# Performance work log

Hardware: AMD Instinct MI355X
Metric: run time of the kernel (lower is better)

Reference implementation:

```python
import jax, jax.numpy as jnp
import numpy as np

T, NE, NA, OBS, D, CH, VH, ITERS = 128, 64, 8, 64, 128, 128, 256, 2
B = NE * NA  # num_actors


def setup_inputs() -> dict:
    key = jax.random.key(0)
    ks = jax.random.split(key, 16)
    rn = lambda k, shape, s=0.05: jax.random.normal(k, shape, jnp.float32) * s
    z = lambda *shape: jnp.zeros(shape, jnp.float32)
    return dict(
        hidden=z(B, D),
        obs=rn(ks[0], (T, B, OBS), 1.0),
        dones=jax.random.bernoulli(ks[1], 0.05, (T, B)),
        embed1_w=rn(ks[2], (OBS, D)), embed1_b=z(D),
        embed2_w=rn(ks[3], (D, D)), embed2_b=z(D),
        gru_Wi=rn(ks[4], (D, 3 * D)), gru_bi=z(3 * D),
        gru_Wh=rn(ks[5], (D, 3 * D)), gru_bhn=z(D),
        couple_h_w=rn(ks[6], (2 * D, CH)), couple_h_b=z(CH),
        couple_out_w=rn(ks[7], (CH, 1)), couple_out_b=z(1),
        update_h_w=rn(ks[8], (2 * D, D)), update_h_b=z(D),
        update_out_w=rn(ks[9], (D, D)), update_out_b=z(D),
        value_h1_w=rn(ks[10], (D, VH)), value_h1_b=z(VH),
        value_h2_w=rn(ks[11], (VH, VH)), value_h2_b=z(VH),
        value_out_w=rn(ks[12], (VH, 1)), value_out_b=z(1),
    )


def _gru_scan(hidden, x, dones, Wi, bi, Wh, bhn):
    # flax GRUCell math: r,z gates (no hidden bias), n gate with hidden bias.
    def step(h, xd):
        xt, dt = xd
        h = jnp.where(dt[:, None], 0.0, h)  # reset carry on done
        gi = xt @ Wi + bi                   # [B, 3D]
        gh = h @ Wh                         # [B, 3D]
        i_r, i_z, i_n = jnp.split(gi, 3, axis=-1)
        h_r, h_z, h_n = jnp.split(gh, 3, axis=-1)
        r = jax.nn.sigmoid(i_r + h_r)
        zg = jax.nn.sigmoid(i_z + h_z)
        n = jnp.tanh(i_n + r * (h_n + bhn))
        new_h = (1.0 - zg) * n + zg * h
        return new_h, new_h
    return jax.lax.scan(step, hidden, (x, dones))


def reference(hidden, obs, dones,
              embed1_w, embed1_b, embed2_w, embed2_b,
              gru_Wi, gru_bi, gru_Wh, gru_bhn,
              couple_h_w, couple_h_b, couple_out_w, couple_out_b,
              update_h_w, update_h_b, update_out_w, update_out_b,
              value_h1_w, value_h1_b, value_h2_w, value_h2_b,
              value_out_w, value_out_b):
    # observation embedding MLP
    emb = jax.nn.relu(obs @ embed1_w + embed1_b)
    emb = jax.nn.relu(emb @ embed2_w + embed2_b)
    hidden, rnn_out = _gru_scan(hidden, emb, dones, gru_Wi, gru_bi, gru_Wh, gru_bhn)

    e = rnn_out.reshape(T, NE, NA, D)
    alive = (1.0 - dones.astype(jnp.float32)).reshape(T, NE, NA)
    e = e * alive[..., None]
    identity_mask = 1.0 - jnp.eye(NA, dtype=jnp.float32)

    # split-linear trick: couple_h(concat[h_i, h_j]) == h_i @ W1 + h_j @ W2 + b
    W1, W2 = couple_h_w[:D], couple_h_w[D:]
    U1, U2 = update_h_w[:D], update_h_w[D:]

    for _ in range(ITERS):
        a_i = jnp.einsum('teid,dh->teih', e, W1)  # [T,E,A,CH]
        a_j = jnp.einsum('tejd,dh->tejh', e, W2)
        Ch = jax.nn.relu(a_i[:, :, :, None, :] + a_j[:, :, None, :, :] + couple_h_b)  # [T,E,A,A,CH]
        C = jax.nn.sigmoid(jnp.einsum('teijh,h->teij', Ch, couple_out_w[:, 0]) + couple_out_b[0])
        C = C * alive[:, :, None, :] * identity_mask[None, None, :, :]
        context = jnp.einsum('teij,tejd->teid', C, e)
        delta = jax.nn.relu(e @ U1 + context @ U2 + update_h_b)
        delta = jax.nn.relu(delta @ update_out_w + update_out_b)
        e = (e + delta) * alive[..., None]

    v = jax.nn.relu(e @ value_h1_w + value_h1_b)
    v = jax.nn.relu(v @ value_h2_w + value_h2_b)
    v = (v @ value_out_w + value_out_b)[..., 0]  # [T,E,A]
    values = v.reshape(T, B)
    return hidden, values
```

## Files before the change

kernel.cpp:

```cpp
#include <hip/hip_runtime.h>
#include <hip/hip_bf16.h>
#include <math.h>

#define T_ 128
#define NE_ 64
#define NA_ 8
#define B_ 512
#define OBS_ 64
#define D_ 128
#define CH_ 128
#define VH_ 256
#define M_ (T_*B_)

typedef __attribute__((ext_vector_type(8))) short bf16x8;
typedef __attribute__((ext_vector_type(8))) _Float16 f16x8;
typedef __attribute__((ext_vector_type(4))) float f32x4;

__device__ __forceinline__ float sigmoidf_(float x){ return 1.f/(1.f+__expf(-x)); }
__device__ __forceinline__ unsigned short f2bu(float v){
  __hip_bfloat16 b = __float2bfloat16(v);
  return __builtin_bit_cast(unsigned short, b);
}
__device__ __forceinline__ float bu2f(unsigned short u){
  return __builtin_bit_cast(float, (unsigned int)u << 16);
}
__device__ __forceinline__ unsigned short f2hu(float v){
  _Float16 h = (_Float16)v;
  return __builtin_bit_cast(unsigned short, h);
}
__device__ __forceinline__ float hu2f(unsigned short u){
  return (float)__builtin_bit_cast(_Float16, u);
}

__global__ __launch_bounds__(256)
void embgi_k(const float* __restrict__ obs,
             const ushort* __restrict__ e1wT, const float* __restrict__ e1b,
             const ushort* __restrict__ e2wT, const float* __restrict__ e2b,
             const ushort* __restrict__ gWiT, const float* __restrict__ gbi,
             ushort* __restrict__ giH)
{
  __shared__ ushort S1[128*136];
  __shared__ ushort S2[128*136];
  const int tid  = threadIdx.x;
  const int lane = tid & 63, wave = tid >> 6;
  const int wm = wave >> 1, wn = wave & 1;
  const int quad = lane >> 4, ln = lane & 15;
  const int m0 = blockIdx.x * 128;

  f32x4 acc[4][4];

  #pragma unroll
  for (int i=0;i<8;i++){
    int c4 = tid + i*256;
    int m = c4 >> 4, kf = (c4 & 15) * 4;
    float4 v = *(const float4*)&obs[(size_t)(m0+m)*OBS_ + kf];
    ushort4 h; h.x=f2hu(v.x); h.y=f2hu(v.y); h.z=f2hu(v.z); h.w=f2hu(v.w);
    *(ushort4*)&S1[m*136 + kf] = h;
  }
  #pragma unroll
  for (int i=0;i<4;i++){
    int c8 = tid + i*256;
    int n = c8 >> 3, kq = (c8 & 7)*8;
    *(uint4*)&S2[n*136 + kq] = *(const uint4*)&e1wT[(size_t)n*64 + kq];
  }
  __syncthreads();

  #pragma unroll
  for (int i=0;i<4;i++)
    #pragma unroll
    for (int j=0;j<4;j++)
      #pragma unroll
      for (int r=0;r<4;r++) acc[i][j][r] = 0.f;
  #pragma unroll
  for (int ks=0; ks<2; ks++){
    const int kq = ks*32 + quad*8;
    f16x8 af[4], bfv[4];
    #pragma unroll
    for (int mt=0;mt<4;mt++)
      af[mt] = *(const f16x8*)&S1[(wm*64 + mt*16 + ln)*136 + kq];
    #pragma unroll
    for (int nt=0;nt<4;nt++)
      bfv[nt] = *(const f16x8*)&S2[(wn*64 + nt*16 + ln)*136 + kq];
    #pragma unroll
    for (int mt=0;mt<4;mt++)
      #pragma unroll
      for (int nt=0;nt<4;nt++)
        acc[mt][nt] = __builtin_amdgcn_mfma_f32_16x16x32_f16(af[mt], bfv[nt], acc[mt][nt], 0,0,0);
  }
  __syncthreads();

  #pragma unroll
  for (int mt=0;mt<4;mt++)
    #pragma unroll
    for (int r=0;r<4;r++){
      int rl = wm*64 + mt*16 + quad*4 + r;
      #pragma unroll
      for (int nt=0;nt<4;nt++){
        int cl = wn*64 + nt*16 + ln;
        S1[rl*136 + cl] = f2hu(fmaxf(acc[mt][nt][r] + e1b[cl], 0.f));
      }
    }
  #pragma unroll
  for (int i=0;i<8;i++){
    int c8 = tid + i*256;
    int n = c8 >> 4, kq = (c8 & 15)*8;
    *(uint4*)&S2[n*136 + kq] = *(const uint4*)&e2wT[(size_t)n*128 + kq];
  }
  __syncthreads();

  #pragma unroll
  for (int i=0;i<4;i++)
    #pragma unroll
    for (int j=0;j<4;j++)
      #pragma unroll
      for (int r=0;r<4;r++) acc[i][j][r] = 0.f;
  #pragma unroll
  for (int ks=0; ks<4; ks++){
    const int kq = ks*32 + quad*8;
    f16x8 af[4], bfv[4];
    #pragma unroll
    for (int mt=0;mt<4;mt++)
      af[mt] = *(const f16x8*)&S1[(wm*64 + mt*16 + ln)*136 + kq];
    #pragma unroll
    for (int nt=0;nt<4;nt++)
      bfv[nt] = *(const f16x8*)&S2[(wn*64 + nt*16 + ln)*136 + kq];
    #pragma unroll
    for (int mt=0;mt<4;mt++)
      #pragma unroll
      for (int nt=0;nt<4;nt++)
        acc[mt][nt] = __builtin_amdgcn_mfma_f32_16x16x32_f16(af[mt], bfv[nt], acc[mt][nt], 0,0,0);
  }
  __syncthreads();

  #pragma unroll
  for (int mt=0;mt<4;mt++)
    #pragma unroll
    for (int r=0;r<4;r++){
      int rl = wm*64 + mt*16 + quad*4 + r;
      #pragma unroll
      for (int nt=0;nt<4;nt++){
        int cl = wn*64 + nt*16 + ln;
        S1[rl*136 + cl] = f2hu(fmaxf(acc[mt][nt][r] + e2b[cl], 0.f));
      }
    }

  for (int c=0; c<3; c++){
    #pragma unroll
    for (int i=0;i<8;i++){
      int c8 = tid + i*256;
      int n = c8 >> 4, kq = (c8 & 15)*8;
      *(uint4*)&S2[n*136 + kq] = *(const uint4*)&gWiT[(size_t)(c*128+n)*128 + kq];
    }
    __syncthreads();
    #pragma unroll
    for (int i=0;i<4;i++)
      #pragma unroll
      for (int j=0;j<4;j++)
        #pragma unroll
        for (int r=0;r<4;r++) acc[i][j][r] = 0.f;
    #pragma unroll
    for (int ks=0; ks<4; ks++){
      const int kq = ks*32 + quad*8;
      f16x8 af[4], bfv[4];
      #pragma unroll
      for (int mt=0;mt<4;mt++)
        af[mt] = *(const f16x8*)&S1[(wm*64 + mt*16 + ln)*136 + kq];
      #pragma unroll
      for (int nt=0;nt<4;nt++)
        bfv[nt] = *(const f16x8*)&S2[(wn*64 + nt*16 + ln)*136 + kq];
      #pragma unroll
      for (int mt=0;mt<4;mt++)
        #pragma unroll
        for (int nt=0;nt<4;nt++)
          acc[mt][nt] = __builtin_amdgcn_mfma_f32_16x16x32_f16(af[mt], bfv[nt], acc[mt][nt], 0,0,0);
    }
    __syncthreads();
    #pragma unroll
    for (int mt=0;mt<4;mt++)
      #pragma unroll
      for (int r=0;r<4;r++){
        int row = m0 + wm*64 + mt*16 + quad*4 + r;
        #pragma unroll
        for (int nt=0;nt<4;nt++){
          int cl = wn*64 + nt*16 + ln;
          giH[(size_t)row*384 + c*128 + cl] = f2hu(acc[mt][nt][r] + gbi[c*128 + cl]);
        }
      }
  }
}

__global__ __launch_bounds__(256, 1)
void upd3_k(const __hip_bfloat16* __restrict__ Xe, const __hip_bfloat16* __restrict__ bcatT,
            const float* __restrict__ chb, const float* __restrict__ cow,
            const float* __restrict__ cob,
            const __hip_bfloat16* __restrict__ uhwT, const float* __restrict__ uhb,
            const __hip_bfloat16* __restrict__ uowT, const float* __restrict__ uob,
            const int* __restrict__ dones, __hip_bfloat16* __restrict__ XeOut)
{
  __shared__ ushort S1[128*136];
  __shared__ ushort Bs[128*136];
  __shared__ ushort XcS[128*136];
  __shared__ alignas(16) float AI[32][132];
  __shared__ alignas(16) float AJ[32][132];
  __shared__ alignas(16) float cbw[CH_], cww[CH_];
  __shared__ float Cs[4][NA_][NA_];
  const int tid  = threadIdx.x;
  const int lane = tid & 63, wave = tid >> 6;
  const int wm = wave >> 1, wn = wave & 1;
  const int quad = lane >> 4, ln = lane & 15;
  const int m0 = blockIdx.x * 128;

  #pragma unroll
  for (int i=0;i<8;i++){
    int c8 = tid + i*256;
    int m = c8 >> 4, kq = (c8 & 15)*8;
    *(uint4*)&S1[m*136 + kq] = *(const uint4*)((const ushort*)Xe + (size_t)(m0+m)*128 + kq);
  }
  if (tid < 128){ cbw[tid] = chb[tid]; cww[tid] = cow[tid]; }
  const float cob0 = cob[0];
  __syncthreads();

  for (int g=0; g<4; g++){
    const int r0 = g*32;
    #pragma unroll
    for (int i=0;i<8;i++){
      int c8 = tid + i*256;
      int n = c8 >> 4, kq = (c8 & 15)*8;
      *(uint4*)&Bs[n*136 + kq] = *(const uint4*)((const ushort*)bcatT + (size_t)n*128 + kq);
    }
    __syncthreads();
    {
      f32x4 acc[2][2];
      #pragma unroll
      for (int mt=0;mt<2;mt++)
        #pragma unroll
        for (int nt=0;nt<2;nt++)
          #pragma unroll
          for (int r=0;r<4;r++) acc[mt][nt][r] = 0.f;
      #pragma unroll
      for (int ks=0; ks<4; ks++){
        const int kq = ks*32 + quad*8;
        bf16x8 af[2], bfv[2];
        #pragma unroll
        for (int mt=0;mt<2;mt++)
          af[mt] = *(const bf16x8*)&S1[(r0 + mt*16 + ln)*136 + kq];
        #pragma unroll
        for (int nt=0;nt<2;nt++)
          bfv[nt] = *(const bf16x8*)&Bs[(wave*32 + nt*16 + ln)*136 + kq];
        #pragma unroll
        for (int mt=0;mt<2;mt++)
          #pragma unroll
          for (int nt=0;nt<2;nt++)
            acc[mt][nt] = __builtin_amdgcn_mfma_f32_16x16x32_bf16(af[mt], bfv[nt], acc[mt][nt], 0,0,0);
      }
      __syncthreads();
      #pragma unroll
      for (int mt=0;mt<2;mt++)
        #pragma unroll
        for (int r=0;r<4;r++)
          #pragma unroll
          for (int nt=0;nt<2;nt++)
            AI[mt*16 + quad*4 + r][wave*32 + nt*16 + ln] = acc[mt][nt][r];
    }
    #pragma unroll
    for (int i=0;i<8;i++){
      int c8 = tid + i*256;
      int n = c8 >> 4, kq = (c8 & 15)*8;
      *(uint4*)&Bs[n*136 + kq] = *(const uint4*)((const ushort*)bcatT + (size_t)(128+n)*128 + kq);
    }
    __syncthreads();
    {
      f32x4 acc[2][2];
      #pragma unroll
      for (int mt=0;mt<2;mt++)
        #pragma unroll
        for (int nt=0;nt<2;nt++)
          #pragma unroll
          for (int r=0;r<4;r++) acc[mt][nt][r] = 0.f;
      #pragma unroll
      for (int ks=0; ks<4; ks++){
        const int kq = ks*32 + quad*8;
        bf16x8 af[2], bfv[2];
        #pragma unroll
        for (int mt=0;mt<2;mt++)
          af[mt] = *(const bf16x8*)&S1[(r0 + mt*16 + ln)*136 + kq];
        #pragma unroll
        for (int nt=0;nt<2;nt++)
          bfv[nt] = *(const bf16x8*)&Bs[(wave*32 + nt*16 + ln)*136 + kq];
        #pragma unroll
        for (int mt=0;mt<2;mt++)
          #pragma unroll
          for (int nt=0;nt<2;nt++)
            acc[mt][nt] = __builtin_amdgcn_mfma_f32_16x16x32_bf16(af[mt], bfv[nt], acc[mt][nt], 0,0,0);
      }
      #pragma unroll
      for (int mt=0;mt<2;mt++)
        #pragma unroll
        for (int r=0;r<4;r++)
          #pragma unroll
          for (int nt=0;nt<2;nt++)
            AJ[mt*16 + quad*4 + r][wave*32 + nt*16 + ln] = acc[mt][nt][r];
    }
    __syncthreads();

    {
      const int env = tid >> 6;
      const int p = tid & 63, i = p >> 3, j = p & 7;
      const float* aiR = &AI[env*8 + i][0];
      const float* ajR = &AJ[env*8 + j][0];
      float s = 0.f;
      #pragma unroll
      for (int h4=0; h4<32; h4++){
        float4 a4 = *(const float4*)&aiR[h4*4];
        float4 b4 = *(const float4*)&ajR[h4*4];
        float4 c4 = *(const float4*)&cbw[h4*4];
        float4 w4 = *(const float4*)&cww[h4*4];
        s += fmaxf(a4.x + b4.x + c4.x, 0.f) * w4.x;
        s += fmaxf(a4.y + b4.y + c4.y, 0.f) * w4.y;
        s += fmaxf(a4.z + b4.z + c4.z, 0.f) * w4.z;
        s += fmaxf(a4.w + b4.w + c4.w, 0.f) * w4.w;
      }
      float Cv = sigmoidf_(s + cob0);
      Cs[env][i][j] = (i==j) ? 0.f : Cv;
    }
    __syncthreads();

    {
      const int lr = tid >> 3;
      const int env = lr >> 3, i = lr & 7;
      const int c0 = (tid & 7) * 16;
      #pragma unroll
      for (int cc=0; cc<4; cc++){
        int d = c0 + cc*4;
        float a0=0.f, a1=0.f, a2=0.f, a3=0.f;
        #pragma unroll
        for (int j=0;j<NA_;j++){
          float c = Cs[env][i][j];
          ushort4 e4 = *(const ushort4*)&S1[(r0 + env*8 + j)*136 + d];
          a0 = fmaf(c, bu2f(e4.x), a0);
          a1 = fmaf(c, bu2f(e4.y), a1);
          a2 = fmaf(c, bu2f(e4.z), a2);
          a3 = fmaf(c, bu2f(e4.w), a3);
        }
        ushort4 o; o.x=f2bu(a0); o.y=f2bu(a1); o.z=f2bu(a2); o.w=f2bu(a3);
        *(ushort4*)&XcS[(r0 + lr)*136 + d] = o;
      }
    }
    __syncthreads();
  }

  f32x4 acc[4][4];
  #pragma unroll
  for (int i=0;i<4;i++)
    #pragma unroll
    for (int j=0;j<4;j++)
      #pragma unroll
      for (int r=0;r<4;r++) acc[i][j][r] = 0.f;

  #pragma unroll
  for (int kc=0; kc<2; kc++){
    #pragma unroll
    for (int i=0;i<8;i++){
      int c8 = tid + i*256;
      int n = c8 >> 4, kq = (c8 & 15)*8;
      *(uint4*)&Bs[n*136 + kq] = *(const uint4*)((const ushort*)uhwT + (size_t)n*256 + kc*128 + kq);
    }
    __syncthreads();
    const ushort* Ab = kc ? XcS : S1;
    #pragma unroll
    for (int ks=0; ks<4; ks++){
      const int kq = ks*32 + quad*8;
      bf16x8 af[4], bfv[4];
      #pragma unroll
      for (int mt=0;mt<4;mt++)
        af[mt] = *(const bf16x8*)&Ab[(wm*64 + mt*16 + ln)*136 + kq];
      #pragma unroll
      for (int nt=0;nt<4;nt++)
        bfv[nt] = *(const bf16x8*)&Bs[(wn*64 + nt*16 + ln)*136 + kq];
      #pragma unroll
      for (int mt=0;mt<4;mt++)
        #pragma unroll
        for (int nt=0;nt<4;nt++)
          acc[mt][nt] = __builtin_amdgcn_mfma_f32_16x16x32_bf16(af[mt], bfv[nt], acc[mt][nt], 0,0,0);
    }
    __syncthreads();
  }

  #pragma unroll
  for (int i=0;i<8;i++){
    int c8 = tid + i*256;
    int n = c8 >> 4, kq = (c8 & 15)*8;
    *(uint4*)&Bs[n*136 + kq] = *(const uint4*)((const ushort*)uowT + (size_t)n*128 + kq);
  }
  #pragma unroll
  for (int mt=0;mt<4;mt++)
    #pragma unroll
    for (int r=0;r<4;r++){
      int rl = wm*64 + mt*16 + quad*4 + r;
      #pragma unroll
      for (int nt=0;nt<4;nt++){
        int cl = wn*64 + nt*16 + ln;
        XcS[rl*136 + cl] = f2bu(fmaxf(acc[mt][nt][r] + uhb[cl], 0.f));
      }
    }
  __syncthreads();

  f32x4 acc2[4][4];
  #pragma unroll
  for (int i=0;i<4;i++)
    #pragma unroll
    for (int j=0;j<4;j++)
      #pragma unroll
      for (int r=0;r<4;r++) acc2[i][j][r] = 0.f;
  #pragma unroll
  for (int ks=0; ks<4; ks++){
    const int kq = ks*32 + quad*8;
    bf16x8 af[4], bfv[4];
    #pragma unroll
    for (int mt=0;mt<4;mt++)
      af[mt] = *(const bf16x8*)&XcS[(wm*64 + mt*16 + ln)*136 + kq];
    #pragma unroll
    for (int nt=0;nt<4;nt++)
      bfv[nt] = *(const bf16x8*)&Bs[(wn*64 + nt*16 + ln)*136 + kq];
    #pragma unroll
    for (int mt=0;mt<4;mt++)
      #pragma unroll
      for (int nt=0;nt<4;nt++)
        acc2[mt][nt] = __builtin_amdgcn_mfma_f32_16x16x32_bf16(af[mt], bfv[nt], acc2[mt][nt], 0,0,0);
  }
  #pragma unroll
  for (int mt=0;mt<4;mt++){
    #pragma unroll
    for (int r=0;r<4;r++){
      int rl = wm*64 + mt*16 + quad*4 + r;
      int row = m0 + rl;
      float al = (dones[row]!=0) ? 0.f : 1.f;
      #pragma unroll
      for (int nt=0;nt<4;nt++){
        int cl = wn*64 + nt*16 + ln;
        float v = fmaxf(acc2[mt][nt][r] + uob[cl], 0.f);
        v += bu2f(S1[rl*136 + cl]);
        v *= al;
        XeOut[(size_t)row*128 + cl] = __float2bfloat16(v);
      }
    }
  }
}

__global__ __launch_bounds__(256)
void vheadf_k(const __hip_bfloat16* __restrict__ Xe, const __hip_bfloat16* __restrict__ v1wT,
              const float* __restrict__ v1b, const __hip_bfloat16* __restrict__ v2wT,
              const float* __restrict__ v2b, const float* __restrict__ vow,
              const float* __restrict__ vob, float* __restrict__ values)
{
  __shared__ ushort S1[128*136];
  __shared__ ushort S2[128*136];
  __shared__ ushort V1[2][128*136];
  const int tid  = threadIdx.x;
  const int lane = tid & 63, wave = tid >> 6;
  const int wm = wave >> 1, wn = wave & 1;
  const int quad = lane >> 4, ln = lane & 15;
  const int m0 = blockIdx.x * 128;

  #pragma unroll
  for (int i=0;i<8;i++){
    int c8 = tid + i*256;
    int m = c8 >> 4, kq = (c8 & 15)*8;
    *(uint4*)&S1[m*136 + kq] = *(const uint4*)((const ushort*)Xe + (size_t)(m0+m)*128 + kq);
  }

  for (int h=0; h<2; h++){
    #pragma unroll
    for (int i=0;i<8;i++){
      int c8 = tid + i*256;
      int n = c8 >> 4, kq = (c8 & 15)*8;
      *(uint4*)&S2[n*136 + kq] = *(const uint4*)((const ushort*)v1wT + (size_t)(h*128+n)*128 + kq);
    }
    __syncthreads();
    f32x4 acc[4][4];
    #pragma unroll
    for (int i=0;i<4;i++)
      #pragma unroll
      for (int j=0;j<4;j++)
        #pragma unroll
        for (int r=0;r<4;r++) acc[i][j][r] = 0.f;
    #pragma unroll
    for (int ks=0; ks<4; ks++){
      const int kq = ks*32 + quad*8;
      bf16x8 af[4], bfv[4];
      #pragma unroll
      for (int mt=0;mt<4;mt++)
        af[mt] = *(const bf16x8*)&S1[(wm*64 + mt*16 + ln)*136 + kq];
      #pragma unroll
      for (int nt=0;nt<4;nt++)
        bfv[nt] = *(const bf16x8*)&S2[(wn*64 + nt*16 + ln)*136 + kq];
      #pragma unroll
      for (int mt=0;mt<4;mt++)
        #pragma unroll
        for (int nt=0;nt<4;nt++)
          acc[mt][nt] = __builtin_amdgcn_mfma_f32_16x16x32_bf16(af[mt], bfv[nt], acc[mt][nt], 0,0,0);
    }
    __syncthreads();
    #pragma unroll
    for (int mt=0;mt<4;mt++)
      #pragma unroll
      for (int r=0;r<4;r++){
        int rl = wm*64 + mt*16 + quad*4 + r;
        #pragma unroll
        for (int nt=0;nt<4;nt++){
          int cl = wn*64 + nt*16 + ln;
          V1[h][rl*136 + cl] = f2bu(fmaxf(acc[mt][nt][r] + v1b[h*128 + cl], 0.f));
        }
      }
  }

  float s[4][4];
  #pragma unroll
  for (int mt=0;mt<4;mt++)
    #pragma unroll
    for (int r=0;r<4;r++) s[mt][r] = 0.f;

  for (int oc=0; oc<2; oc++){
    f32x4 acc[4][4];
    #pragma unroll
    for (int i=0;i<4;i++)
      #pragma unroll
      for (int j=0;j<4;j++)
        #pragma unroll
        for (int r=0;r<4;r++) acc[i][j][r] = 0.f;
    for (int kh=0; kh<2; kh++){
      #pragma unroll
      for (int i=0;i<8;i++){
        int c8 = tid + i*256;
        int n = c8 >> 4, kq = (c8 & 15)*8;
        *(uint4*)&S2[n*136 + kq] = *(const uint4*)((const ushort*)v2wT + (size_t)(oc*128+n)*256 + kh*128 + kq);
      }
      __syncthreads();
      #pragma unroll
      for (int ks=0; ks<4; ks++){
        const int kq = ks*32 + quad*8;
        bf16x8 af[4], bfv[4];
        #pragma unroll
        for (int mt=0;mt<4;mt++)
          af[mt] = *(const bf16x8*)&V1[kh][(wm*64 + mt*16 + ln)*136 + kq];
        #pragma unroll
        for (int nt=0;nt<4;nt++)
          bfv[nt] = *(const bf16x8*)&S2[(wn*64 + nt*16 + ln)*136 + kq];
        #pragma unroll
        for (int mt=0;mt<4;mt++)
          #pragma unroll
          for (int nt=0;nt<4;nt++)
            acc[mt][nt] = __builtin_amdgcn_mfma_f32_16x16x32_bf16(af[mt], bfv[nt], acc[mt][nt], 0,0,0);
      }
      __syncthreads();
    }
    float v2bv[4], voww[4];
    #pragma unroll
    for (int nt=0;nt<4;nt++){
      int col = oc*128 + wn*64 + nt*16 + ln;
      v2bv[nt] = v2b[col];
      voww[nt] = vow[col];
    }
    #pragma unroll
    for (int mt=0;mt<4;mt++)
      #pragma unroll
      for (int r=0;r<4;r++){
        float p = 0.f;
        #pragma unroll
        for (int nt=0;nt<4;nt++)
          p += fmaxf(acc[mt][nt][r] + v2bv[nt], 0.f) * voww[nt];
        s[mt][r] += p;
      }
  }

  #pragma unroll
  for (int off=1; off<16; off<<=1)
    #pragma unroll
    for (int mt=0;mt<4;mt++)
      #pragma unroll
      for (int r=0;r<4;r++)
        s[mt][r] += __shfl_xor(s[mt][r], off);
  if (ln == 0){
    float add = (wn == 0) ? vob[0] : 0.f;
    #pragma unroll
    for (int mt=0;mt<4;mt++)
      #pragma unroll
      for (int r=0;r<4;r++)
        atomicAdd(&values[m0 + wm*64 + mt*16 + quad*4 + r], s[mt][r] + add);
  }
}

__global__ __launch_bounds__(512, 1)
void grum8_k(const ushort* __restrict__ gih, const float* __restrict__ hidden0,
             const int* __restrict__ dones, const float* __restrict__ gWh,
             const float* __restrict__ bhn, __hip_bfloat16* __restrict__ eb_out,
             float* __restrict__ hout)
{
  __shared__ ushort wstg[32*392];
  __shared__ ushort hb[2][16*136];
  __shared__ float  dnS[T_*4];
  const int tid  = threadIdx.x;
  const int lane = tid & 63, wave = tid >> 6;
  const int quad = lane >> 4, ln = lane & 15;
  const int r0   = blockIdx.x * 4;
  const int col  = wave*16 + ln;
  const int lnb  = ln & 12;

  dnS[tid] = (dones[(size_t)(tid>>2)*B_ + r0 + (tid&3)] != 0) ? 1.f : 0.f;
  const float bhnr = bhn[col];

  for (int i=tid; i<16*136; i+=512){ hb[0][i]=0; hb[1][i]=0; }

  f16x8 bf[3][4];
  #pragma unroll
  for (int kc=0; kc<4; kc++){
    for (int i=tid; i<32*384; i+=512){
      int kk = i/384, c = i - kk*384;
      wstg[kk*392 + c] = f2hu(gWh[(size_t)(kc*32+kk)*384 + c]);
    }
    __syncthreads();
    #pragma unroll
    for (int g=0; g<3; g++){
      int c = g*128 + col;
      ushort tmp[8];
      #pragma unroll
      for (int j=0;j<8;j++) tmp[j] = wstg[(quad*8+j)*392 + c];
      bf[g][kc] = *(const f16x8*)tmp;
    }
    __syncthreads();
  }

  float hc = hidden0[(size_t)(r0+quad)*D_ + col];
  if (dnS[quad] > 0.5f) hc = 0.f;
  hb[0][(quad*4)*136 + col] = f2hu(hc);
  __syncthreads();

  const ushort* gbase = gih + ((size_t)(r0+quad))*384;
  const size_t  gstep = (size_t)B_*384;

  float c_r, c_z, c_n;
  c_r = hu2f(gbase[col]); c_z = hu2f(gbase[col+128]); c_n = hu2f(gbase[col+256]);
  ushort aR,aZ,aN, bR,bZ,bN, cR,cZ,cN, dR,dZ,dN;
  { const ushort* gp = gbase + 1*gstep; aR = gp[col]; aZ = gp[col+128]; aN = gp[col+256]; }
  { const ushort* gp = gbase + 2*gstep; bR = gp[col]; bZ = gp[col+128]; bN = gp[col+256]; }
  { const ushort* gp = gbase + 3*gstep; cR = gp[col]; cZ = gp[col+128]; cN = gp[col+256]; }
  dR=0; dZ=0; dN=0;

  ushort pend_eu = 0;

#define GSTEP(t, IR,IZ,IN, OR,OZ,ON)                                          \
  {                                                                           \
    if ((t) > 0)                                                              \
      ((ushort*)eb_out)[((size_t)((t)-1)*B_ + r0+quad)*D_ + col] = pend_eu;   \
    { int tl = (t)+4; if (tl > T_-1) tl = T_-1;                               \
      const ushort* gp = gbase + (size_t)tl*gstep;                            \
      OR = gp[col]; OZ = gp[col+128]; ON = gp[col+256]; }                     \
    const ushort* hbuf = hb[(t)&1];                                           \
    f32x4 accA[3], accB[3];                                                   \
    _Pragma("unroll")                                                         \
    for (int g=0;g<3;g++){                                                    \
      _Pragma("unroll")                                                       \
      for (int r=0;r<4;r++){ accA[g][r]=0.f; accB[g][r]=0.f; }                \
    }                                                                         \
    _Pragma("unroll")                                                         \
    for (int ks=0; ks<2; ks++){                                               \
      f16x8 ahA = *(const f16x8*)&hbuf[lnb*136 + (2*ks  )*32 + quad*8];       \
      f16x8 ahB = *(const f16x8*)&hbuf[lnb*136 + (2*ks+1)*32 + quad*8];       \
      _Pragma("unroll")                                                       \
      for (int g=0;g<3;g++){                                                  \
        accA[g] = __builtin_amdgcn_mfma_f32_16x16x32_f16(ahA, bf[g][2*ks  ], accA[g], 0,0,0); \
        accB[g] = __builtin_amdgcn_mfma_f32_16x16x32_f16(ahB, bf[g][2*ks+1], accB[g], 0,0,0); \
      }                                                                       \
    }                                                                         \
    const float dnow  = dnS[(t)*4 + quad];                                    \
    const float dnext = ((t)+1 < T_) ? dnS[((t)+1)*4 + quad] : 0.f;           \
    float rg = sigmoidf_(c_r + accA[0][0] + accB[0][0]);                      \
    float zg = sigmoidf_(c_z + accA[1][0] + accB[1][0]);                      \
    float x  = c_n + rg*(accA[2][0] + accB[2][0] + bhnr);                     \
    float ng = 2.f/(1.f+__expf(-2.f*x)) - 1.f;                                \
    float hnew = (1.f - zg)*ng + zg*hc;                                       \
    pend_eu = f2bu(hnew*(1.f-dnow));                                          \
    float hv = (dnext > 0.5f) ? 0.f : hnew;                                   \
    hc = hv;                                                                  \
    hb[((t)+1)&1][(quad*4)*136 + col] = f2hu(hv);                             \
    asm volatile("s_waitcnt lgkmcnt(0)\n\ts_barrier" ::: "memory");           \
    c_r = hu2f(IR); c_z = hu2f(IZ); c_n = hu2f(IN);                           \
  }

  for (int t=0; t<T_; t+=4){
    GSTEP(t+0, aR,aZ,aN, dR,dZ,dN);
    GSTEP(t+1, bR,bZ,bN, aR,aZ,aN);
    GSTEP(t+2, cR,cZ,cN, bR,bZ,bN);
    GSTEP(t+3, dR,dZ,dN, cR,cZ,cN);
  }
#undef GSTEP

  ((ushort*)eb_out)[((size_t)(T_-1)*B_ + r0+quad)*D_ + col] = pend_eu;
  hout[(size_t)(r0+quad)*D_ + col] = hc;
}

__global__ __launch_bounds__(256)
void packall_k(const float* __restrict__ e1w, ushort* __restrict__ e1T,
               const float* __restrict__ e2w, ushort* __restrict__ e2T,
               const float* __restrict__ gWi, ushort* __restrict__ giT,
               const float* __restrict__ chw, __hip_bfloat16* __restrict__ bcatT,
               const float* __restrict__ uhw, __hip_bfloat16* __restrict__ uhwT,
               const float* __restrict__ uow, __hip_bfloat16* __restrict__ uowT,
               const float* __restrict__ v1w, __hip_bfloat16* __restrict__ v1wT,
               const float* __restrict__ v2w, __hip_bfloat16* __restrict__ v2wT)
{
  const int b = blockIdx.x, tid = threadIdx.x;
  if (b < 32){
    int idx = b*256 + tid;
    int n = idx >> 6, k = idx & 63;
    e1T[idx] = f2hu(e1w[k*128 + n]);
  } else if (b < 96){
    int idx = (b-32)*256 + tid;
    int n = idx >> 7, k = idx & 127;
    e2T[idx] = f2hu(e2w[k*128 + n]);
  } else if (b < 288){
    int idx = (b-96)*256 + tid;
    int n = idx >> 7, k = idx & 127;
    giT[idx] = f2hu(gWi[k*384 + n]);
  } else if (b < 416){
    int idx = (b-288)*256 + tid;
    int n = idx >> 7, k = idx & 127;
    float v = (n < 128) ? chw[k*128 + n] : chw[(128+k)*128 + (n-128)];
    bcatT[idx] = __float2bfloat16(v);
  } else if (b < 544){
    int idx = (b-416)*256 + tid;
    int r = idx >> 7, c = idx & 127;
    uhwT[c*256 + r] = __float2bfloat16(uhw[idx]);
  } else if (b < 608){
    int idx = (b-544)*256 + tid;
    int r = idx >> 7, c = idx & 127;
    uowT[c*128 + r] = __float2bfloat16(uow[idx]);
  } else if (b < 736){
    int idx = (b-608)*256 + tid;
    int r = idx >> 8, c = idx & 255;
    v1wT[c*128 + r] = __float2bfloat16(v1w[idx]);
  } else {
    int idx = (b-736)*256 + tid;
    int r = idx >> 8, c = idx & 255;
    v2wT[c*256 + r] = __float2bfloat16(v2w[idx]);
  }
}

extern "C" void kernel_launch(void* const* d_in, const int* in_sizes, int n_in,
                              void* d_out, int out_size, void* d_ws, size_t ws_size,
                              hipStream_t stream) {
  const float* hidden = (const float*)d_in[0];
  const float* obs    = (const float*)d_in[1];
  const int*   dones  = (const int*)  d_in[2];
  const float* e1w = (const float*)d_in[3];
  const float* e1b = (const float*)d_in[4];
  const float* e2w = (const float*)d_in[5];
  const float* e2b = (const float*)d_in[6];
  const float* gWi = (const float*)d_in[7];
  const float* gbi = (const float*)d_in[8];
  const float* gWh = (const float*)d_in[9];
  const float* gbhn= (const float*)d_in[10];
  const float* chw = (const float*)d_in[11];
  const float* chb = (const float*)d_in[12];
  const float* cow = (const float*)d_in[13];
  const float* cob = (const float*)d_in[14];
  const float* uhw = (const float*)d_in[15];
  const float* uhb = (const float*)d_in[16];
  const float* uow = (const float*)d_in[17];
  const float* uob = (const float*)d_in[18];
  const float* v1w = (const float*)d_in[19];
  const float* v1b = (const float*)d_in[20];
  const float* v2w = (const float*)d_in[21];
  const float* v2b = (const float*)d_in[22];
  const float* vow = (const float*)d_in[23];
  const float* vob = (const float*)d_in[24];
  (void)in_sizes; (void)n_in; (void)out_size;

  float* out_hidden = (float*)d_out;
  float* out_values = (float*)d_out + (size_t)B_*D_;

  float* ws = (float*)d_ws;
  ushort* giH   = (ushort*)(ws + 10485760);
  __hip_bfloat16* Xe = (__hip_bfloat16*)(ws + 23068672);
  ushort* wb    = (ushort*)(ws + 27262976);
  if (ws_size < (size_t)27500000 * sizeof(float)) return;

  __hip_bfloat16* bcatT = (__hip_bfloat16*)wb;
  __hip_bfloat16* uhwT  = (__hip_bfloat16*)wb + 32768;
  __hip_bfloat16* uowT  = (__hip_bfloat16*)wb + 65536;
  __hip_bfloat16* v1wT  = (__hip_bfloat16*)wb + 81920;
  __hip_bfloat16* v2wT  = (__hip_bfloat16*)wb + 114688;
  ushort* e1wT = wb + 180224;
  ushort* e2wT = wb + 188416;
  ushort* gWiT = wb + 204800;

  dim3 blk(256);
  hipMemsetAsync(out_values, 0, (size_t)M_*sizeof(float), stream);
  packall_k<<<dim3(992), blk, 0, stream>>>(
    e1w, e1wT, e2w, e2wT, gWi, gWiT,
    chw, bcatT, uhw, uhwT, uow, uowT, v1w, v1wT, v2w, v2wT);

  embgi_k<<<dim3(512), blk, 0, stream>>>(obs, e1wT, e1b, e2wT, e2b, gWiT, gbi, giH);

  grum8_k<<<dim3(128), dim3(512), 0, stream>>>(giH, hidden, dones, gWh, gbhn, Xe, out_hidden);

  for (int it=0; it<2; it++){
    upd3_k<<<dim3(512), blk, 0, stream>>>(Xe, bcatT, chb, cow, cob,
                                          uhwT, uhb, uowT, uob, dones, Xe);
  }
  vheadf_k<<<dim3(512), blk, 0, stream>>>(Xe, v1wT, v1b, v2wT, v2b, vow, vob, out_values);
}
```

Baseline: 359.9 us.

## Fuse both message-passing iterations and value head into one kernel

Merges the two upd3_k launches and the vheadf_k launch into a single postgru_k kernel. Each block keeps its 128-row entity tile resident in LDS across both iterations and the value head, so the intermediate Xe tensor no longer round-trips through global memory. Shared memory is reorganized into a pooled buffer aliased between XcS/AI/AJ and V1 to fit. The risk is higher LDS footprint and register pressure, and the kernel still pays for two launches' worth of work in a single launch of 512 blocks.

```diff
diff --git a/kernel.cpp b/kernel.cpp
--- a/kernel.cpp
+++ b/kernel.cpp
@@ -190,18 +190,20 @@
 }
 
 __global__ __launch_bounds__(256, 1)
-void upd3_k(const __hip_bfloat16* __restrict__ Xe, const __hip_bfloat16* __restrict__ bcatT,
-            const float* __restrict__ chb, const float* __restrict__ cow,
-            const float* __restrict__ cob,
-            const __hip_bfloat16* __restrict__ uhwT, const float* __restrict__ uhb,
-            const __hip_bfloat16* __restrict__ uowT, const float* __restrict__ uob,
-            const int* __restrict__ dones, __hip_bfloat16* __restrict__ XeOut)
+void postgru_k(const __hip_bfloat16* __restrict__ Xe, const __hip_bfloat16* __restrict__ bcatT,
+               const float* __restrict__ chb, const float* __restrict__ cow,
+               const float* __restrict__ cob,
+               const __hip_bfloat16* __restrict__ uhwT, const float* __restrict__ uhb,
+               const __hip_bfloat16* __restrict__ uowT, const float* __restrict__ uob,
+               const int* __restrict__ dones,
+               const __hip_bfloat16* __restrict__ v1wT, const float* __restrict__ v1b,
+               const __hip_bfloat16* __restrict__ v2wT, const float* __restrict__ v2b,
+               const float* __restrict__ vow, const float* __restrict__ vob,
+               float* __restrict__ values)
 {
   __shared__ ushort S1[128*136];
   __shared__ ushort Bs[128*136];
-  __shared__ ushort XcS[128*136];
-  __shared__ alignas(16) float AI[32][132];
-  __shared__ alignas(16) float AJ[32][132];
+  __shared__ alignas(16) ushort Pool[2*128*136];
   __shared__ alignas(16) float cbw[CH_], cww[CH_];
   __shared__ float Cs[4][NA_][NA_];
   const int tid  = threadIdx.x;
@@ -210,6 +212,10 @@
   const int quad = lane >> 4, ln = lane & 15;
   const int m0 = blockIdx.x * 128;
 
+  ushort* XcS = Pool;
+  float (*AI)[132] = (float(*)[132])(Pool + 128*136);
+  float (*AJ)[132] = (float(*)[132])((char*)(Pool + 128*136) + 16896);
+
   #pragma unroll
   for (int i=0;i<8;i++){
     int c8 = tid + i*256;
@@ -220,160 +226,259 @@
   const float cob0 = cob[0];
   __syncthreads();
 
-  for (int g=0; g<4; g++){
-    const int r0 = g*32;
+  for (int it=0; it<2; it++){
+    for (int g=0; g<4; g++){
+      const int r0 = g*32;
+      #pragma unroll
+      for (int i=0;i<8;i++){
+        int c8 = tid + i*256;
+        int n = c8 >> 4, kq = (c8 & 15)*8;
+        *(uint4*)&Bs[n*136 + kq] = *(const uint4*)((const ushort*)bcatT + (size_t)n*128 + kq);
+      }
+      __syncthreads();
+      {
+        f32x4 acc[2][2];
+        #pragma unroll
+        for (int mt=0;mt<2;mt++)
+          #pragma unroll
+          for (int nt=0;nt<2;nt++)
+            #pragma unroll
+            for (int r=0;r<4;r++) acc[mt][nt][r] = 0.f;
+        #pragma unroll
+        for (int ks=0; ks<4; ks++){
+          const int kq = ks*32 + quad*8;
+          bf16x8 af[2], bfv[2];
+          #pragma unroll
+          for (int mt=0;mt<2;mt++)
+            af[mt] = *(const bf16x8*)&S1[(r0 + mt*16 + ln)*136 + kq];
+          #pragma unroll
+          for (int nt=0;nt<2;nt++)
+            bfv[nt] = *(const bf16x8*)&Bs[(wave*32 + nt*16 + ln)*136 + kq];
+          #pragma unroll
+          for (int mt=0;mt<2;mt++)
+            #pragma unroll
+            for (int nt=0;nt<2;nt++)
+              acc[mt][nt] = __builtin_amdgcn_mfma_f32_16x16x32_bf16(af[mt], bfv[nt], acc[mt][nt], 0,0,0);
+        }
+        __syncthreads();
+        #pragma unroll
+        for (int mt=0;mt<2;mt++)
+          #pragma unroll
+          for (int r=0;r<4;r++)
+            #pragma unroll
+            for (int nt=0;nt<2;nt++)
+              AI[mt*16 + quad*4 + r][wave*32 + nt*16 + ln] = acc[mt][nt][r];
+      }
+      #pragma unroll
+      for (int i=0;i<8;i++){
+        int c8 = tid + i*256;
+        int n = c8 >> 4, kq = (c8 & 15)*8;
+        *(uint4*)&Bs[n*136 + kq] = *(const uint4*)((const ushort*)bcatT + (size_t)(128+n)*128 + kq);
+      }
+      __syncthreads();
+      {
+        f32x4 acc[2][2];
+        #pragma unroll
+        for (int mt=0;mt<2;mt++)
+          #pragma unroll
+          for (int nt=0;nt<2;nt++)
+            #pragma unroll
+            for (int r=0;r<4;r++) acc[mt][nt][r] = 0.f;
+        #pragma unroll
+        for (int ks=0; ks<4; ks++){
+          const int kq = ks*32 + quad*8;
+          bf16x8 af[2], bfv[2];
+          #pragma unroll
+          for (int mt=0;mt<2;mt++)
+            af[mt] = *(const bf16x8*)&S1[(r0 + mt*16 + ln)*136 + kq];
+          #pragma unroll
+          for (int nt=0;nt<2;nt++)
+            bfv[nt] = *(const bf16x8*)&Bs[(wave*32 + nt*16 + ln)*136 + kq];
+          #pragma unroll
+          for (int mt=0;mt<2;mt++)
+            #pragma unroll
+            for (int nt=0;nt<2;nt++)
+              acc[mt][nt] = __builtin_amdgcn_mfma_f32_16x16x32_bf16(af[mt], bfv[nt], acc[mt][nt], 0,0,0);
+        }
+        #pragma unroll
+        for (int mt=0;mt<2;mt++)
+          #pragma unroll
+          for (int r=0;r<4;r++)
+            #pragma unroll
+            for (int nt=0;nt<2;nt++)
+              AJ[mt*16 + quad*4 + r][wave*32 + nt*16 + ln] = acc[mt][nt][r];
+      }
+      __syncthreads();
+
+      {
+        const int env = tid >> 6;
+        const int p = tid & 63, i = p >> 3, j = p & 7;
+        const float* aiR = &AI[env*8 + i][0];
+        const float* ajR = &AJ[env*8 + j][0];
+        float s = 0.f;
+        #pragma unroll
+        for (int h4=0; h4<32; h4++){
+          float4 a4 = *(const float4*)&aiR[h4*4];
+          float4 b4 = *(const float4*)&ajR[h4*4];
+          float4 c4 = *(const float4*)&cbw[h4*4];
+          float4 w4 = *(const float4*)&cww[h4*4];
+          s += fmaxf(a4.x + b4.x + c4.x, 0.f) * w4.x;
+          s += fmaxf(a4.y + b4.y + c4.y, 0.f) * w4.y;
+          s += fmaxf(a4.z + b4.z + c4.z, 0.f) * w4.z;
+          s += fmaxf(a4.w + b4.w + c4.w, 0.f) * w4.w;
+        }
+        float Cv = sigmoidf_(s + cob0);
+        Cs[env][i][j] = (i==j) ? 0.f : Cv;
+      }
+      __syncthreads();
+
+      {
+        const int lr = tid >> 3;
+        const int env = lr >> 3, i = lr & 7;
+        const int c0 = (tid & 7) * 16;
+        #pragma unroll
+        for (int cc=0; cc<4; cc++){
+          int d = c0 + cc*4;
+          float a0=0.f, a1=0.f, a2=0.f, a3=0.f;
+          #pragma unroll
+          for (int j=0;j<NA_;j++){
+            float c = Cs[env][i][j];
+            ushort4 e4 = *(const ushort4*)&S1[(r0 + env*8 + j)*136 + d];
+            a0 = fmaf(c, bu2f(e4.x), a0);
+            a1 = fmaf(c, bu2f(e4.y), a1);
+            a2 = fmaf(c, bu2f(e4.z), a2);
+            a3 = fmaf(c, bu2f(e4.w), a3);
+          }
+          ushort4 o; o.x=f2bu(a0); o.y=f2bu(a1); o.z=f2bu(a2); o.w=f2bu(a3);
+          *(ushort4*)&XcS[(r0 + lr)*136 + d] = o;
+        }
+      }
+      __syncthreads();
+    }
+
+    f32x4 acc[4][4];
+    #pragma unroll
+    for (int i=0;i<4;i++)
+      #pragma unroll
+      for (int j=0;j<4;j++)
+        #pragma unroll
+        for (int r=0;r<4;r++) acc[i][j][r] = 0.f;
+
+    #pragma unroll
+    for (int kc=0; kc<2; kc++){
+      #pragma unroll
+      for (int i=0;i<8;i++){
+        int c8 = tid + i*256;
+        int n = c8 >> 4, kq = (c8 & 15)*8;
+        *(uint4*)&Bs[n*136 + kq] = *(const uint4*)((const ushort*)uhwT + (size_t)n*256 + kc*128 + kq);
+      }
+      __syncthreads();
+      const ushort* Ab = kc ? XcS : S1;
+      #pragma unroll
+      for (int ks=0; ks<4; ks++){
+        const int kq = ks*32 + quad*8;
+        bf16x8 af[4], bfv[4];
+        #pragma unroll
+        for (int mt=0;mt<4;mt++)
+          af[mt] = *(const bf16x8*)&Ab[(wm*64 + mt*16 + ln)*136 + kq];
+        #pragma unroll
+        for (int nt=0;nt<4;nt++)
+          bfv[nt] = *(const bf16x8*)&Bs[(wn*64 + nt*16 + ln)*136 + kq];
+        #pragma unroll
+        for (int mt=0;mt<4;mt++)
+          #pragma unroll
+          for (int nt=0;nt<4;nt++)
+            acc[mt][nt] = __builtin_amdgcn_mfma_f32_16x16x32_bf16(af[mt], bfv[nt], acc[mt][nt], 0,0,0);
+      }
+      __syncthreads();
+    }
+
     #pragma unroll
     for (int i=0;i<8;i++){
       int c8 = tid + i*256;
       int n = c8 >> 4, kq = (c8 & 15)*8;
-      *(uint4*)&Bs[n*136 + kq] = *(const uint4*)((const ushort*)bcatT + (size_t)n*128 + kq);
-    }
+      *(uint4*)&Bs[n*136 + kq] = *(const uint4*)((const ushort*)uowT + (size_t)n*128 + kq);
+    }
+    #pragma unroll
+    for (int mt=0;mt<4;mt++)
+      #pragma unroll
+      for (int r=0;r<4;r++){
+        int rl = wm*64 + mt*16 + quad*4 + r;
+        #pragma unroll
+        for (int nt=0;nt<4;nt++){
+          int cl = wn*64 + nt*16 + ln;
+          XcS[rl*136 + cl] = f2bu(fmaxf(acc[mt][nt][r] + uhb[cl], 0.f));
+        }
+      }
     __syncthreads();
-    {
-      f32x4 acc[2][2];
-      #pragma unroll
-      for (int mt=0;mt<2;mt++)
-        #pragma unroll
-        for (int nt=0;nt<2;nt++)
-          #pragma unroll
-          for (int r=0;r<4;r++) acc[mt][nt][r] = 0.f;
-      #pragma unroll
-      for (int ks=0; ks<4; ks++){
-        const int kq = ks*32 + quad*8;
-        bf16x8 af[2], bfv[2];
-        #pragma unroll
-        for (int mt=0;mt<2;mt++)
-          af[mt] = *(const bf16x8*)&S1[(r0 + mt*16 + ln)*136 + kq];
-        #pragma unroll
-        for (int nt=0;nt<2;nt++)
-          bfv[nt] = *(const bf16x8*)&Bs[(wave*32 + nt*16 + ln)*136 + kq];
-        #pragma unroll
-        for (int mt=0;mt<2;mt++)
-          #pragma unroll
-          for (int nt=0;nt<2;nt++)
-            acc[mt][nt] = __builtin_amdgcn_mfma_f32_16x16x32_bf16(af[mt], bfv[nt], acc[mt][nt], 0,0,0);
-      }
-      __syncthreads();
-      #pragma unroll
-      for (int mt=0;mt<2;mt++)
-        #pragma unroll
-        for (int r=0;r<4;r++)
-          #pragma unroll
-          for (int nt=0;nt<2;nt++)
-            AI[mt*16 + quad*4 + r][wave*32 + nt*16 + ln] = acc[mt][nt][r];
-    }
+
+    f32x4 acc2[4][4];
+    #pragma unroll
+    for (int i=0;i<4;i++)
+      #pragma unroll
+      for (int j=0;j<4;j++)
+        #pragma unroll
+        for (int r=0;r<4;r++) acc2[i][j][r] = 0.f;
+    #pragma unroll
+    for (int ks=0; ks<4; ks++){
+      const int kq = ks*32 + quad*8;
+      bf16x8 af[4], bfv[4];
+      #pragma unroll
+      for (int mt=0;mt<4;mt++)
+        af[mt] = *(const bf16x8*)&XcS[(wm*64 + mt*16 + ln)*136 + kq];
+      #pragma unroll
+      for (int nt=0;nt<4;nt++)
+        bfv[nt] = *(const bf16x8*)&Bs[(wn*64 + nt*16 + ln)*136 + kq];
+      #pragma unroll
+      for (int mt=0;mt<4;mt++)
+        #pragma unroll
+        for (int nt=0;nt<4;nt++)
+          acc2[mt][nt] = __builtin_amdgcn_mfma_f32_16x16x32_bf16(af[mt], bfv[nt], acc2[mt][nt], 0,0,0);
+    }
+    #pragma unroll
+    for (int mt=0;mt<4;mt++){
+      #pragma unroll
+      for (int r=0;r<4;r++){
+        int rl = wm*64 + mt*16 + quad*4 + r;
+        int row = m0 + rl;
+        float al = (dones[row]!=0) ? 0.f : 1.f;
+        #pragma unroll
+        for (int nt=0;nt<4;nt++){
+          int cl = wn*64 + nt*16 + ln;
+          float v = fmaxf(acc2[mt][nt][r] + uob[cl], 0.f);
+          v += bu2f(S1[rl*136 + cl]);
+          v *= al;
+          S1[rl*136 + cl] = f2bu(v);
+        }
+      }
+    }
+    __syncthreads();
+  }
+
+  ushort* V1 = Pool;
+
+  for (int h=0; h<2; h++){
     #pragma unroll
     for (int i=0;i<8;i++){
       int c8 = tid + i*256;
       int n = c8 >> 4, kq = (c8 & 15)*8;
-      *(uint4*)&Bs[n*136 + kq] = *(const uint4*)((const ushort*)bcatT + (size_t)(128+n)*128 + kq);
+      *(uint4*)&Bs[n*136 + kq] = *(const uint4*)((const ushort*)v1wT + (size_t)(h*128+n)*128 + kq);
     }
     __syncthreads();
-    {
-      f32x4 acc[2][2];
-      #pragma unroll
-      for (int mt=0;mt<2;mt++)
-        #pragma unroll
-        for (int nt=0;nt<2;nt++)
-          #pragma unroll
-          for (int r=0;r<4;r++) acc[mt][nt][r] = 0.f;
-      #pragma unroll
-      for (int ks=0; ks<4; ks++){
-        const int kq = ks*32 + quad*8;
-        bf16x8 af[2], bfv[2];
-        #pragma unroll
-        for (int mt=0;mt<2;mt++)
-          af[mt] = *(const bf16x8*)&S1[(r0 + mt*16 + ln)*136 + kq];
-        #pragma unroll
-        for (int nt=0;nt<2;nt++)
-          bfv[nt] = *(const bf16x8*)&Bs[(wave*32 + nt*16 + ln)*136 + kq];
-        #pragma unroll
-        for (int mt=0;mt<2;mt++)
-          #pragma unroll
-          for (int nt=0;nt<2;nt++)
-            acc[mt][nt] = __builtin_amdgcn_mfma_f32_16x16x32_bf16(af[mt], bfv[nt], acc[mt][nt], 0,0,0);
-      }
-      #pragma unroll
-      for (int mt=0;mt<2;mt++)
-        #pragma unroll
-        for (int r=0;r<4;r++)
-          #pragma unroll
-          for (int nt=0;nt<2;nt++)
-            AJ[mt*16 + quad*4 + r][wave*32 + nt*16 + ln] = acc[mt][nt][r];
-    }
-    __syncthreads();
-
-    {
-      const int env = tid >> 6;
-      const int p = tid & 63, i = p >> 3, j = p & 7;
-      const float* aiR = &AI[env*8 + i][0];
-      const float* ajR = &AJ[env*8 + j][0];
-      float s = 0.f;
-      #pragma unroll
-      for (int h4=0; h4<32; h4++){
-        float4 a4 = *(const float4*)&aiR[h4*4];
-        float4 b4 = *(const float4*)&ajR[h4*4];
-        float4 c4 = *(const float4*)&cbw[h4*4];
-        float4 w4 = *(const float4*)&cww[h4*4];
-        s += fmaxf(a4.x + b4.x + c4.x, 0.f) * w4.x;
-        s += fmaxf(a4.y + b4.y + c4.y, 0.f) * w4.y;
-        s += fmaxf(a4.z + b4.z + c4.z, 0.f) * w4.z;
-        s += fmaxf(a4.w + b4.w + c4.w, 0.f) * w4.w;
-      }
-      float Cv = sigmoidf_(s + cob0);
-      Cs[env][i][j] = (i==j) ? 0.f : Cv;
-    }
-    __syncthreads();
-
-    {
-      const int lr = tid >> 3;
-      const int env = lr >> 3, i = lr & 7;
-      const int c0 = (tid & 7) * 16;
-      #pragma unroll
-      for (int cc=0; cc<4; cc++){
-        int d = c0 + cc*4;
-        float a0=0.f, a1=0.f, a2=0.f, a3=0.f;
-        #pragma unroll
-        for (int j=0;j<NA_;j++){
-          float c = Cs[env][i][j];
-          ushort4 e4 = *(const ushort4*)&S1[(r0 + env*8 + j)*136 + d];
-          a0 = fmaf(c, bu2f(e4.x), a0);
-          a1 = fmaf(c, bu2f(e4.y), a1);
-          a2 = fmaf(c, bu2f(e4.z), a2);
-          a3 = fmaf(c, bu2f(e4.w), a3);
-        }
-        ushort4 o; o.x=f2bu(a0); o.y=f2bu(a1); o.z=f2bu(a2); o.w=f2bu(a3);
-        *(ushort4*)&XcS[(r0 + lr)*136 + d] = o;
-      }
-    }
-    __syncthreads();
-  }
-
-  f32x4 acc[4][4];
-  #pragma unroll
-  for (int i=0;i<4;i++)
-    #pragma unroll
-    for (int j=0;j<4;j++)
-      #pragma unroll
-      for (int r=0;r<4;r++) acc[i][j][r] = 0.f;
-
-  #pragma unroll
-  for (int kc=0; kc<2; kc++){
-    #pragma unroll
-    for (int i=0;i<8;i++){
-      int c8 = tid + i*256;
-      int n = c8 >> 4, kq = (c8 & 15)*8;
-      *(uint4*)&Bs[n*136 + kq] = *(const uint4*)((const ushort*)uhwT + (size_t)n*256 + kc*128 + kq);
-    }
-    __syncthreads();
-    const ushort* Ab = kc ? XcS : S1;
+    f32x4 acc[4][4];
+    #pragma unroll
+    for (int i=0;i<4;i++)
+      #pragma unroll
+      for (int j=0;j<4;j++)
+        #pragma unroll
+        for (int r=0;r<4;r++) acc[i][j][r] = 0.f;
     #pragma unroll
     for (int ks=0; ks<4; ks++){
       const int kq = ks*32 + quad*8;
       bf16x8 af[4], bfv[4];
       #pragma unroll
       for (int mt=0;mt<4;mt++)
-        af[mt] = *(const bf16x8*)&Ab[(wm*64 + mt*16 + ln)*136 + kq];
+        af[mt] = *(const bf16x8*)&S1[(wm*64 + mt*16 + ln)*136 + kq];
       #pragma unroll
       for (int nt=0;nt<4;nt++)
         bfv[nt] = *(const bf16x8*)&Bs[(wn*64 + nt*16 + ln)*136 + kq];
@@ -384,123 +489,6 @@
           acc[mt][nt] = __builtin_amdgcn_mfma_f32_16x16x32_bf16(af[mt], bfv[nt], acc[mt][nt], 0,0,0);
     }
     __syncthreads();
-  }
-
-  #pragma unroll
-  for (int i=0;i<8;i++){
-    int c8 = tid + i*256;
-    int n = c8 >> 4, kq = (c8 & 15)*8;
-    *(uint4*)&Bs[n*136 + kq] = *(const uint4*)((const ushort*)uowT + (size_t)n*128 + kq);
-  }
-  #pragma unroll
-  for (int mt=0;mt<4;mt++)
-    #pragma unroll
-    for (int r=0;r<4;r++){
-      int rl = wm*64 + mt*16 + quad*4 + r;
-      #pragma unroll
-      for (int nt=0;nt<4;nt++){
-        int cl = wn*64 + nt*16 + ln;
-        XcS[rl*136 + cl] = f2bu(fmaxf(acc[mt][nt][r] + uhb[cl], 0.f));
-      }
-    }
-  __syncthreads();
-
-  f32x4 acc2[4][4];
-  #pragma unroll
-  for (int i=0;i<4;i++)
-    #pragma unroll
-    for (int j=0;j<4;j++)
-      #pragma unroll
-      for (int r=0;r<4;r++) acc2[i][j][r] = 0.f;
-  #pragma unroll
-  for (int ks=0; ks<4; ks++){
-    const int kq = ks*32 + quad*8;
-    bf16x8 af[4], bfv[4];
-    #pragma unroll
-    for (int mt=0;mt<4;mt++)
-      af[mt] = *(const bf16x8*)&XcS[(wm*64 + mt*16 + ln)*136 + kq];
-    #pragma unroll
-    for (int nt=0;nt<4;nt++)
-      bfv[nt] = *(const bf16x8*)&Bs[(wn*64 + nt*16 + ln)*136 + kq];
-    #pragma unroll
-    for (int mt=0;mt<4;mt++)
-      #pragma unroll
-      for (int nt=0;nt<4;nt++)
-        acc2[mt][nt] = __builtin_amdgcn_mfma_f32_16x16x32_bf16(af[mt], bfv[nt], acc2[mt][nt], 0,0,0);
-  }
-  #pragma unroll
-  for (int mt=0;mt<4;mt++){
-    #pragma unroll
-    for (int r=0;r<4;r++){
-      int rl = wm*64 + mt*16 + quad*4 + r;
-      int row = m0 + rl;
-      float al = (dones[row]!=0) ? 0.f : 1.f;
-      #pragma unroll
-      for (int nt=0;nt<4;nt++){
-        int cl = wn*64 + nt*16 + ln;
-        float v = fmaxf(acc2[mt][nt][r] + uob[cl], 0.f);
-        v += bu2f(S1[rl*136 + cl]);
-        v *= al;
-        XeOut[(size_t)row*128 + cl] = __float2bfloat16(v);
-      }
-    }
-  }
-}
-
-__global__ __launch_bounds__(256)
-void vheadf_k(const __hip_bfloat16* __restrict__ Xe, const __hip_bfloat16* __restrict__ v1wT,
-              const float* __restrict__ v1b, const __hip_bfloat16* __restrict__ v2wT,
-              const float* __restrict__ v2b, const float* __restrict__ vow,
-              const float* __restrict__ vob, float* __restrict__ values)
-{
-  __shared__ ushort S1[128*136];
-  __shared__ ushort S2[128*136];
-  __shared__ ushort V1[2][128*136];
-  const int tid  = threadIdx.x;
-  const int lane = tid & 63, wave = tid >> 6;
-  const int wm = wave >> 1, wn = wave & 1;
-  const int quad = lane >> 4, ln = lane & 15;
-  const int m0 = blockIdx.x * 128;
-
-  #pragma unroll
-  for (int i=0;i<8;i++){
-    int c8 = tid + i*256;
-    int m = c8 >> 4, kq = (c8 & 15)*8;
-    *(uint4*)&S1[m*136 + kq] = *(const uint4*)((const ushort*)Xe + (size_t)(m0+m)*128 + kq);
-  }
-
-  for (int h=0; h<2; h++){
-    #pragma unroll
-    for (int i=0;i<8;i++){
-      int c8 = tid + i*256;
-      int n = c8 >> 4, kq = (c8 & 15)*8;
-      *(uint4*)&S2[n*136 + kq] = *(const uint4*)((const ushort*)v1wT + (size_t)(h*128+n)*128 + kq);
-    }
-    __syncthreads();
-    f32x4 acc[4][4];
-    #pragma unroll
-    for (int i=0;i<4;i++)
-      #pragma unroll
-      for (int j=0;j<4;j++)
-        #pragma unroll
-        for (int r=0;r<4;r++) acc[i][j][r] = 0.f;
-    #pragma unroll
-    for (int ks=0; ks<4; ks++){
-      const int kq = ks*32 + quad*8;
-      bf16x8 af[4], bfv[4];
-      #pragma unroll
-      for (int mt=0;mt<4;mt++)
-        af[mt] = *(const bf16x8*)&S1[(wm*64 + mt*16 + ln)*136 + kq];
-      #pragma unroll
-      for (int nt=0;nt<4;nt++)
-        bfv[nt] = *(const bf16x8*)&S2[(wn*64 + nt*16 + ln)*136 + kq];
-      #pragma unroll
-      for (int mt=0;mt<4;mt++)
-        #pragma unroll
-        for (int nt=0;nt<4;nt++)
-          acc[mt][nt] = __builtin_amdgcn_mfma_f32_16x16x32_bf16(af[mt], bfv[nt], acc[mt][nt], 0,0,0);
-    }
-    __syncthreads();
     #pragma unroll
     for (int mt=0;mt<4;mt++)
       #pragma unroll
@@ -509,7 +497,7 @@
         #pragma unroll
         for (int nt=0;nt<4;nt++){
           int cl = wn*64 + nt*16 + ln;
-          V1[h][rl*136 + cl] = f2bu(fmaxf(acc[mt][nt][r] + v1b[h*128 + cl], 0.f));
+          V1[h*128*136 + rl*136 + cl] = f2bu(fmaxf(acc[mt][nt][r] + v1b[h*128 + cl], 0.f));
         }
       }
   }
@@ -533,7 +521,7 @@
       for (int i=0;i<8;i++){
         int c8 = tid + i*256;
         int n = c8 >> 4, kq = (c8 & 15)*8;
-        *(uint4*)&S2[n*136 + kq] = *(const uint4*)((const ushort*)v2wT + (size_t)(oc*128+n)*256 + kh*128 + kq);
+        *(uint4*)&Bs[n*136 + kq] = *(const uint4*)((const ushort*)v2wT + (size_t)(oc*128+n)*256 + kh*128 + kq);
       }
       __syncthreads();
       #pragma unroll
@@ -542,10 +530,10 @@
         bf16x8 af[4], bfv[4];
         #pragma unroll
         for (int mt=0;mt<4;mt++)
-          af[mt] = *(const bf16x8*)&V1[kh][(wm*64 + mt*16 + ln)*136 + kq];
+          af[mt] = *(const bf16x8*)&V1[kh*128*136 + (wm*64 + mt*16 + ln)*136 + kq];
         #pragma unroll
         for (int nt=0;nt<4;nt++)
-          bfv[nt] = *(const bf16x8*)&S2[(wn*64 + nt*16 + ln)*136 + kq];
+          bfv[nt] = *(const bf16x8*)&Bs[(wn*64 + nt*16 + ln)*136 + kq];
         #pragma unroll
         for (int mt=0;mt<4;mt++)
           #pragma unroll
@@ -804,9 +792,7 @@
 
   grum8_k<<<dim3(128), dim3(512), 0, stream>>>(giH, hidden, dones, gWh, gbhn, Xe, out_hidden);
 
-  for (int it=0; it<2; it++){
-    upd3_k<<<dim3(512), blk, 0, stream>>>(Xe, bcatT, chb, cow, cob,
-                                          uhwT, uhb, uowT, uob, dones, Xe);
-  }
-  vheadf_k<<<dim3(512), blk, 0, stream>>>(Xe, v1wT, v1b, v2wT, v2b, vow, vob, out_values);
-}
+  postgru_k<<<dim3(512), blk, 0, stream>>>(Xe, bcatT, chb, cow, cob,
+                                           uhwT, uhb, uowT, uob, dones,
+                                           v1wT, v1b, v2wT, v2b, vow, vob, out_values);
+}
```

New measurement: 362.3 us. No clear change (+0.6%).
